# Optimization experiments

Hardware: AMD Instinct MI355X
Metric: run time of the kernel (lower is better)

The kernel has to match this reference:

```python
import jax, jax.numpy as jnp
import numpy as np

N, E, D, L = 50000, 600000, 128, 3  # nodes, edges, feature dim, GIN layers
BN_EPS = 1e-5


def setup_inputs() -> dict:
    key = jax.random.key(0)
    ks = jax.random.split(key, 10)
    x = jax.random.normal(ks[0], (N, D), jnp.float32)
    edge_index = jax.random.randint(ks[1], (2, E), 0, N, jnp.int32)
    s = 1.0 / np.sqrt(D).astype(np.float32)
    W1 = jax.random.uniform(ks[2], (L, D, D), jnp.float32, -s, s)
    b1 = jax.random.uniform(ks[3], (L, D), jnp.float32, -s, s)
    W2 = jax.random.uniform(ks[4], (L, D, D), jnp.float32, -s, s)
    b2 = jax.random.uniform(ks[5], (L, D), jnp.float32, -s, s)
    gamma = jnp.ones((L, D), jnp.float32)
    beta = jnp.zeros((L, D), jnp.float32)
    fc_w = jax.random.uniform(ks[6], (D, 1), jnp.float32, -s, s)
    fc_b = jax.random.uniform(ks[7], (1,), jnp.float32, -s, s)
    return dict(x=x, edge_index=edge_index, W1=W1, b1=b1, W2=W2, b2=b2,
                gamma=gamma, beta=beta, fc_w=fc_w, fc_b=fc_b)


def reference(x, edge_index, W1, b1, W2, b2, gamma, beta, fc_w, fc_b):
    src, dst = edge_index[0], edge_index[1]
    h = x
    for l in range(L):
        # GINConv (eps=0): MLP(x_i + sum_{j->i} x_j)  -- gather then scatter-add
        agg = jax.ops.segment_sum(h[src], dst, num_segments=N)  # [N, D]
        z = h + agg
        z = jax.nn.relu(z @ W1[l] + b1[l]) @ W2[l] + b2[l]  # 2-layer MLP
        # BatchNorm1d (training mode: batch stats, biased variance)
        mu = z.mean(axis=0)
        var = z.var(axis=0)
        z = (z - mu) * jax.lax.rsqrt(var + BN_EPS) * gamma[l] + beta[l]
        h = jax.nn.relu(z)
    return h @ fc_w + fc_b  # [N, 1] per-node q-values
```

## Files before the change

### kernel.cpp

```cpp
#include <hip/hip_runtime.h>
#include <math.h>

#define NN 50000
#define NE 600000
#define DIM 128
#define LAYERS 3
#define BN_EPS 1e-5f

__global__ void k_init(int* __restrict__ deg, float* __restrict__ bnstats) {
    int i = blockIdx.x * 256 + threadIdx.x;
    if (i < NN) deg[i] = 0;
    if (i < LAYERS * 2 * DIM) bnstats[i] = 0.0f;
}

__global__ void k_hist(const int* __restrict__ dst, int* __restrict__ deg) {
    int e = blockIdx.x * 256 + threadIdx.x;
    if (e < NE) atomicAdd(&deg[dst[e]], 1);
}

__global__ void k_scan(const int* __restrict__ deg, int* __restrict__ off) {
    __shared__ int buf[1024];
    __shared__ int carry_s;
    const int t = threadIdx.x;
    if (t == 0) { carry_s = 0; off[0] = 0; }
    __syncthreads();
    for (int base = 0; base < NN; base += 1024) {
        int v = (base + t < NN) ? deg[base + t] : 0;
        buf[t] = v;
        __syncthreads();
        for (int s = 1; s < 1024; s <<= 1) {
            int add = (t >= s) ? buf[t - s] : 0;
            __syncthreads();
            buf[t] += add;
            __syncthreads();
        }
        if (base + t < NN) off[base + t + 1] = carry_s + buf[t];
        __syncthreads();
        if (t == 0) carry_s += buf[1023];
        __syncthreads();
    }
}

__global__ void k_copy(const int* __restrict__ off, int* __restrict__ cur) {
    int i = blockIdx.x * 256 + threadIdx.x;
    if (i < NN) cur[i] = off[i];
}

__global__ void k_fill(const int* __restrict__ src, const int* __restrict__ dst,
                       int* __restrict__ cur, int* __restrict__ csr) {
    int e = blockIdx.x * 256 + threadIdx.x;
    if (e < NE) {
        int p = atomicAdd(&cur[dst[e]], 1);
        csr[p] = src[e];
    }
}

__global__ __launch_bounds__(256) void k_agg(const float* __restrict__ h,
                                             const int* __restrict__ off,
                                             const int* __restrict__ csr,
                                             float* __restrict__ z) {
    int wid  = (blockIdx.x * 256 + threadIdx.x) >> 6;
    int lane = threadIdx.x & 63;
    if (wid >= NN) return;
    const int start = off[wid], end = off[wid + 1];
    float2 acc = *(const float2*)&h[(size_t)wid * DIM + lane * 2];
    int i = start;
    for (; i + 1 < end; i += 2) {
        int s0 = csr[i], s1 = csr[i + 1];
        float2 v0 = *(const float2*)&h[(size_t)s0 * DIM + lane * 2];
        float2 v1 = *(const float2*)&h[(size_t)s1 * DIM + lane * 2];
        acc.x += v0.x + v1.x;
        acc.y += v0.y + v1.y;
    }
    if (i < end) {
        int s0 = csr[i];
        float2 v0 = *(const float2*)&h[(size_t)s0 * DIM + lane * 2];
        acc.x += v0.x;
        acc.y += v0.y;
    }
    *(float2*)&z[(size_t)wid * DIM + lane * 2] = acc;
}

#define TM 32
__global__ __launch_bounds__(256, 2) void k_mlp(float* __restrict__ z,
                                                const float* __restrict__ W1,
                                                const float* __restrict__ b1,
                                                const float* __restrict__ W2,
                                                const float* __restrict__ b2,
                                                float* __restrict__ bnsum,
                                                float* __restrict__ bnsq) {
    __shared__ float zt[TM][DIM];
    __shared__ float w[DIM][DIM];
    const int t = threadIdx.x;
    const int c = t & 31;
    const int r = t >> 5;
    const int row0 = blockIdx.x * TM;

    #pragma unroll
    for (int i = 0; i < 4; ++i) {
        int f4 = t + i * 256;
        int rr = f4 >> 5, c4 = f4 & 31;
        int g  = row0 + rr;
        float4 v = make_float4(0.f, 0.f, 0.f, 0.f);
        if (g < NN) v = *(const float4*)&z[(size_t)g * DIM + c4 * 4];
        *(float4*)&zt[rr][c4 * 4] = v;
    }
    #pragma unroll
    for (int i = 0; i < 16; ++i) {
        int f4 = t + i * 256;
        int k = f4 >> 5, j4 = f4 & 31;
        *(float4*)&w[k][j4 * 4] = *(const float4*)&W1[k * DIM + j4 * 4];
    }
    __syncthreads();

    float acc[4][4];
    #pragma unroll
    for (int i = 0; i < 4; ++i)
        #pragma unroll
        for (int j = 0; j < 4; ++j) acc[i][j] = 0.0f;

    for (int k = 0; k < DIM; k += 4) {
        float4 a4[4];
        #pragma unroll
        for (int i = 0; i < 4; ++i) a4[i] = *(const float4*)&zt[r * 4 + i][k];
        #pragma unroll
        for (int kk = 0; kk < 4; ++kk) {
            const float4 b = *(const float4*)&w[k + kk][c * 4];
            #pragma unroll
            for (int i = 0; i < 4; ++i) {
                const float a = (&a4[i].x)[kk];
                acc[i][0] = fmaf(a, b.x, acc[i][0]);
                acc[i][1] = fmaf(a, b.y, acc[i][1]);
                acc[i][2] = fmaf(a, b.z, acc[i][2]);
                acc[i][3] = fmaf(a, b.w, acc[i][3]);
            }
        }
    }
    __syncthreads();

    const float4 bias1 = *(const float4*)&b1[c * 4];
    #pragma unroll
    for (int i = 0; i < 4; ++i) {
        float4 y;
        y.x = fmaxf(acc[i][0] + bias1.x, 0.f);
        y.y = fmaxf(acc[i][1] + bias1.y, 0.f);
        y.z = fmaxf(acc[i][2] + bias1.z, 0.f);
        y.w = fmaxf(acc[i][3] + bias1.w, 0.f);
        *(float4*)&zt[r * 4 + i][c * 4] = y;
    }
    #pragma unroll
    for (int i = 0; i < 16; ++i) {
        int f4 = t + i * 256;
        int k = f4 >> 5, j4 = f4 & 31;
        *(float4*)&w[k][j4 * 4] = *(const float4*)&W2[k * DIM + j4 * 4];
    }
    __syncthreads();

    #pragma unroll
    for (int i = 0; i < 4; ++i)
        #pragma unroll
        for (int j = 0; j < 4; ++j) acc[i][j] = 0.0f;

    for (int k = 0; k < DIM; k += 4) {
        float4 a4[4];
        #pragma unroll
        for (int i = 0; i < 4; ++i) a4[i] = *(const float4*)&zt[r * 4 + i][k];
        #pragma unroll
        for (int kk = 0; kk < 4; ++kk) {
            const float4 b = *(const float4*)&w[k + kk][c * 4];
            #pragma unroll
            for (int i = 0; i < 4; ++i) {
                const float a = (&a4[i].x)[kk];
                acc[i][0] = fmaf(a, b.x, acc[i][0]);
                acc[i][1] = fmaf(a, b.y, acc[i][1]);
                acc[i][2] = fmaf(a, b.z, acc[i][2]);
                acc[i][3] = fmaf(a, b.w, acc[i][3]);
            }
        }
    }
    __syncthreads();

    const float4 bias2 = *(const float4*)&b2[c * 4];
    float s[4] = {0.f, 0.f, 0.f, 0.f};
    float q[4] = {0.f, 0.f, 0.f, 0.f};
    #pragma unroll
    for (int i = 0; i < 4; ++i) {
        int g = row0 + r * 4 + i;
        float4 zv;
        zv.x = acc[i][0] + bias2.x;
        zv.y = acc[i][1] + bias2.y;
        zv.z = acc[i][2] + bias2.z;
        zv.w = acc[i][3] + bias2.w;
        if (g < NN) {
            *(float4*)&z[(size_t)g * DIM + c * 4] = zv;
            s[0] += zv.x; s[1] += zv.y; s[2] += zv.z; s[3] += zv.w;
            q[0] += zv.x * zv.x; q[1] += zv.y * zv.y;
            q[2] += zv.z * zv.z; q[3] += zv.w * zv.w;
        }
    }
    float* scratch = &zt[0][0];
    #pragma unroll
    for (int j = 0; j < 4; ++j) {
        scratch[r * DIM + c * 4 + j]        = s[j];
        scratch[1024 + r * DIM + c * 4 + j] = q[j];
    }
    __syncthreads();
    if (t < DIM) {
        float ss = 0.f, qq = 0.f;
        #pragma unroll
        for (int rr = 0; rr < 8; ++rr) {
            ss += scratch[rr * DIM + t];
            qq += scratch[1024 + rr * DIM + t];
        }
        atomicAdd(&bnsum[t], ss);
        atomicAdd(&bnsq[t], qq);
    }
}

__global__ __launch_bounds__(256) void k_norm(const float* __restrict__ z,
                                              const float* __restrict__ bnsum,
                                              const float* __restrict__ bnsq,
                                              const float* __restrict__ gamma,
                                              const float* __restrict__ beta,
                                              float* __restrict__ h) {
    int f4 = blockIdx.x * 256 + threadIdx.x;
    if (f4 >= NN * DIM / 4) return;
    int c0 = (f4 & 31) * 4;
    const float invN = 1.0f / (float)NN;
    float sc[4], sh[4];
    #pragma unroll
    for (int j = 0; j < 4; ++j) {
        int col = c0 + j;
        float mu  = bnsum[col] * invN;
        float var = bnsq[col] * invN - mu * mu;
        float k   = rsqrtf(var + BN_EPS) * gamma[col];
        sc[j] = k;
        sh[j] = beta[col] - mu * k;
    }
    float4 v = *(const float4*)&z[(size_t)f4 * 4];
    float4 o;
    o.x = fmaxf(fmaf(v.x, sc[0], sh[0]), 0.f);
    o.y = fmaxf(fmaf(v.y, sc[1], sh[1]), 0.f);
    o.z = fmaxf(fmaf(v.z, sc[2], sh[2]), 0.f);
    o.w = fmaxf(fmaf(v.w, sc[3], sh[3]), 0.f);
    *(float4*)&h[(size_t)f4 * 4] = o;
}

__global__ __launch_bounds__(256) void k_fc(const float* __restrict__ h,
                                            const float* __restrict__ fc_w,
                                            const float* __restrict__ fc_b,
                                            float* __restrict__ out) {
    int wid  = (blockIdx.x * 256 + threadIdx.x) >> 6;
    int lane = threadIdx.x & 63;
    if (wid >= NN) return;
    float2 v = *(const float2*)&h[(size_t)wid * DIM + lane * 2];
    float2 wv = *(const float2*)&fc_w[lane * 2];
    float s = v.x * wv.x + v.y * wv.y;
    #pragma unroll
    for (int o = 32; o >= 1; o >>= 1) s += __shfl_down(s, o);
    if (lane == 0) out[wid] = s + fc_b[0];
}

extern "C" void kernel_launch(void* const* d_in, const int* in_sizes, int n_in,
                              void* d_out, int out_size, void* d_ws, size_t ws_size,
                              hipStream_t stream) {
    const float* x     = (const float*)d_in[0];
    const int*   src   = (const int*)d_in[1];
    const int*   dst   = ((const int*)d_in[1]) + NE;
    const float* W1    = (const float*)d_in[2];
    const float* b1    = (const float*)d_in[3];
    const float* W2    = (const float*)d_in[4];
    const float* b2    = (const float*)d_in[5];
    const float* gamma = (const float*)d_in[6];
    const float* beta  = (const float*)d_in[7];
    const float* fc_w  = (const float*)d_in[8];
    const float* fc_b  = (const float*)d_in[9];
    float* out = (float*)d_out;

    char* ws = (char*)d_ws;
    size_t o = 0;
    auto carve = [&](size_t bytes) {
        char* p = ws + o;
        o += (bytes + 15) & ~(size_t)15;
        return p;
    };
    int*   deg     = (int*)carve(NN * 4);
    int*   off     = (int*)carve((NN + 1) * 4);
    int*   cur     = (int*)carve(NN * 4);
    int*   csr     = (int*)carve(NE * 4);
    float* bnstats = (float*)carve(LAYERS * 2 * DIM * 4);
    float* zbuf    = (float*)carve((size_t)NN * DIM * 4);
    float* h0      = (float*)carve((size_t)NN * DIM * 4);
    float* h1      = (float*)carve((size_t)NN * DIM * 4);

    k_init<<<(NN + 255) / 256, 256, 0, stream>>>(deg, bnstats);
    k_hist<<<(NE + 255) / 256, 256, 0, stream>>>(dst, deg);
    k_scan<<<1, 1024, 0, stream>>>(deg, off);
    k_copy<<<(NN + 255) / 256, 256, 0, stream>>>(off, cur);
    k_fill<<<(NE + 255) / 256, 256, 0, stream>>>(src, dst, cur, csr);

    const float* hin = x;
    float* hbuf[2] = {h0, h1};
    const int nblk_mlp  = (NN + TM - 1) / TM;
    const int nblk_agg  = (NN * 64 + 255) / 256;
    const int nblk_norm = (NN * DIM / 4 + 255) / 256;

    for (int l = 0; l < LAYERS; ++l) {
        float* hout = hbuf[l & 1];
        k_agg<<<nblk_agg, 256, 0, stream>>>(hin, off, csr, zbuf);
        k_mlp<<<nblk_mlp, 256, 0, stream>>>(zbuf,
                                            W1 + (size_t)l * DIM * DIM, b1 + l * DIM,
                                            W2 + (size_t)l * DIM * DIM, b2 + l * DIM,
                                            bnstats + l * DIM,
                                            bnstats + LAYERS * DIM + l * DIM);
        k_norm<<<nblk_norm, 256, 0, stream>>>(zbuf,
                                              bnstats + l * DIM,
                                              bnstats + LAYERS * DIM + l * DIM,
                                              gamma + l * DIM, beta + l * DIM, hout);
        hin = hout;
    }

    k_fc<<<(NN * 64 + 255) / 256, 256, 0, stream>>>(hin, fc_w, fc_b, out);
}
```

Baseline: 655.1 us.

## Replace single-block serial degree scan with multi-block wave-shuffle scan

The CSR offset prefix sum over node degrees was computed by one 1024-thread block looping over all nodes with many block barriers. It is replaced by a three-stage scan: per-block wave-shuffle scans over 2048 elements, a single-wave scan of the block totals, and a fix-up pass that also writes the cursor copy. This spreads the scan across the GPU and removes the long serial barrier chain, at the cost of one extra launch and a small temporary buffer.

```diff
diff --git a/kernel.cpp b/kernel.cpp
--- a/kernel.cpp
+++ b/kernel.cpp
@@ -7,6 +7,9 @@
 #define LAYERS 3
 #define BN_EPS 1e-5f
 
+#define SC_ELE 2048
+#define NSCAN ((NN + SC_ELE - 1) / SC_ELE)
+
 __global__ void k_init(int* __restrict__ deg, float* __restrict__ bnstats) {
     int i = blockIdx.x * 256 + threadIdx.x;
     if (i < NN) deg[i] = 0;
@@ -18,32 +21,62 @@
     if (e < NE) atomicAdd(&deg[dst[e]], 1);
 }
 
-__global__ void k_scan(const int* __restrict__ deg, int* __restrict__ off) {
-    __shared__ int buf[1024];
-    __shared__ int carry_s;
-    const int t = threadIdx.x;
-    if (t == 0) { carry_s = 0; off[0] = 0; }
-    __syncthreads();
-    for (int base = 0; base < NN; base += 1024) {
-        int v = (base + t < NN) ? deg[base + t] : 0;
-        buf[t] = v;
-        __syncthreads();
-        for (int s = 1; s < 1024; s <<= 1) {
-            int add = (t >= s) ? buf[t - s] : 0;
-            __syncthreads();
-            buf[t] += add;
-            __syncthreads();
-        }
-        if (base + t < NN) off[base + t + 1] = carry_s + buf[t];
-        __syncthreads();
-        if (t == 0) carry_s += buf[1023];
-        __syncthreads();
-    }
-}
-
-__global__ void k_copy(const int* __restrict__ off, int* __restrict__ cur) {
+__global__ __launch_bounds__(1024) void k_scan1(const int* __restrict__ deg,
+                                                int* __restrict__ part,
+                                                int* __restrict__ bsum) {
+    __shared__ int ws[16];
+    const int t = threadIdx.x, lane = t & 63, wv = t >> 6;
+    const int base = blockIdx.x * SC_ELE;
+    const int e0 = base + 2 * t, e1 = e0 + 1;
+    const int v0 = (e0 < NN) ? deg[e0] : 0;
+    const int v1 = (e1 < NN) ? deg[e1] : 0;
+    const int s = v0 + v1;
+    int incl = s;
+    #pragma unroll
+    for (int o = 1; o < 64; o <<= 1) {
+        int u = __shfl_up(incl, o);
+        if (lane >= o) incl += u;
+    }
+    if (lane == 63) ws[wv] = incl;
+    __syncthreads();
+    if (wv == 0) {
+        int x = (lane < 16) ? ws[lane] : 0;
+        int ix = x;
+        #pragma unroll
+        for (int o = 1; o < 16; o <<= 1) {
+            int u = __shfl_up(ix, o);
+            if (lane >= o) ix += u;
+        }
+        if (lane < 16) ws[lane] = ix - x;
+        if (lane == 15) bsum[blockIdx.x] = ix;
+    }
+    __syncthreads();
+    const int excl = incl - s + ws[wv];
+    if (e0 < NN) part[e0] = excl;
+    if (e1 < NN) part[e1] = excl + v0;
+}
+
+__global__ void k_scan2(const int* __restrict__ bsum, int* __restrict__ boff) {
+    const int lane = threadIdx.x;
+    const int v = (lane < NSCAN) ? bsum[lane] : 0;
+    int ix = v;
+    #pragma unroll
+    for (int o = 1; o < 64; o <<= 1) {
+        int u = __shfl_up(ix, o);
+        if (lane >= o) ix += u;
+    }
+    if (lane < NSCAN) boff[lane] = ix - v;
+}
+
+__global__ void k_scan3(const int* __restrict__ part, const int* __restrict__ boff,
+                        int* __restrict__ off, int* __restrict__ cur) {
     int i = blockIdx.x * 256 + threadIdx.x;
-    if (i < NN) cur[i] = off[i];
+    if (i < NN) {
+        int o = part[i] + boff[i >> 11];
+        off[i] = o;
+        cur[i] = o;
+        if (i == 0) off[NN] = NE;
+    }
 }
 
 __global__ void k_fill(const int* __restrict__ src, const int* __restrict__ dst,
@@ -288,6 +321,9 @@
     int*   off     = (int*)carve((NN + 1) * 4);
     int*   cur     = (int*)carve(NN * 4);
     int*   csr     = (int*)carve(NE * 4);
+    int*   part    = (int*)carve(NN * 4);
+    int*   bsum    = (int*)carve(NSCAN * 4);
+    int*   boff    = (int*)carve(NSCAN * 4);
     float* bnstats = (float*)carve(LAYERS * 2 * DIM * 4);
     float* zbuf    = (float*)carve((size_t)NN * DIM * 4);
     float* h0      = (float*)carve((size_t)NN * DIM * 4);
@@ -295,8 +331,9 @@
 
     k_init<<<(NN + 255) / 256, 256, 0, stream>>>(deg, bnstats);
     k_hist<<<(NE + 255) / 256, 256, 0, stream>>>(dst, deg);
-    k_scan<<<1, 1024, 0, stream>>>(deg, off);
-    k_copy<<<(NN + 255) / 256, 256, 0, stream>>>(off, cur);
+    k_scan1<<<NSCAN, 1024, 0, stream>>>(deg, part, bsum);
+    k_scan2<<<1, 64, 0, stream>>>(bsum, boff);
+    k_scan3<<<(NN + 255) / 256, 256, 0, stream>>>(part, boff, off, cur);
     k_fill<<<(NE + 255) / 256, 256, 0, stream>>>(src, dst, cur, csr);
 
     const float* hin = x;
```

After: 572.1 us. 1.14x faster.
